# Kernel tuning notes

Hardware: AMD Instinct MI355X
Metric: run time of the kernel (lower is better)

The kernel has to match this reference:

```python
import jax, jax.numpy as jnp
import numpy as np

N_NODES = 200000
N_EDGES = 400000
N_FEAT = 78
DIM = 128
N_LAYERS = 5
N_GRAPHS = 8192
BN_EPS = 1e-5


def setup_inputs() -> dict:
    key = jax.random.key(0)
    ks = jax.random.split(key, 20)
    s = 0.05
    inp = {
        "x": jax.random.normal(ks[0], (N_NODES, N_FEAT), dtype=jnp.float32),
        "edge_index": jax.random.randint(ks[1], (2, N_EDGES), 0, N_NODES, dtype=jnp.int64),
        "batch": jnp.sort(jax.random.randint(ks[2], (N_NODES,), 0, N_GRAPHS, dtype=jnp.int64)),
        "percent": 0,
        # ini_embed: Linear(F,D), ReLU, Linear(D,D)
        "ini_w1": jax.random.normal(ks[3], (N_FEAT, DIM), dtype=jnp.float32) * s,
        "ini_b1": jnp.zeros((DIM,), dtype=jnp.float32),
        "ini_w2": jax.random.normal(ks[4], (DIM, DIM), dtype=jnp.float32) * s,
        "ini_b2": jnp.zeros((DIM,), dtype=jnp.float32),
        # per-layer GIN MLPs (stacked over layers)
        "gin_w1": jax.random.normal(ks[5], (N_LAYERS, DIM, DIM), dtype=jnp.float32) * s,
        "gin_b1": jnp.zeros((N_LAYERS, DIM), dtype=jnp.float32),
        "gin_w2": jax.random.normal(ks[6], (N_LAYERS, DIM, DIM), dtype=jnp.float32) * s,
        "gin_b2": jnp.zeros((N_LAYERS, DIM), dtype=jnp.float32),
        # BatchNorm1d params per layer
        "bn_gamma": jnp.ones((N_LAYERS, DIM), dtype=jnp.float32),
        "bn_beta": jnp.zeros((N_LAYERS, DIM), dtype=jnp.float32),
        # layer_conv: Conv2d(L, 1, (1,1)) == weighted sum over layer axis + scalar bias
        "lc_w": jax.random.normal(ks[7], (N_LAYERS,), dtype=jnp.float32) * s,
        "lc_b": jnp.zeros((), dtype=jnp.float32),
    }
    return inp


def reference(x, edge_index, batch, percent, ini_w1, ini_b1, ini_w2, ini_b2,
              gin_w1, gin_b1, gin_w2, gin_b2, bn_gamma, bn_beta, lc_w, lc_b):
    # ini_embed
    h = jax.nn.relu(x @ ini_w1 + ini_b1) @ ini_w2 + ini_b2  # [N, D]
    src, dst = edge_index[0], edge_index[1]

    layer_outs = []
    for i in range(N_LAYERS):
        # GINConv (eps=0): mlp(x_i + sum_{j->i} x_j)
        agg = jax.ops.segment_sum(h[src], dst, num_segments=N_NODES)  # scatter-add
        z = agg + h
        z = jax.nn.relu(z @ gin_w1[i] + gin_b1[i]) @ gin_w2[i] + gin_b2[i]
        z = jax.nn.relu(z)
        # BatchNorm1d (training-mode batch stats over nodes)
        mean = jnp.mean(z, axis=0)
        var = jnp.var(z, axis=0)
        z = (z - mean) * jax.lax.rsqrt(var + BN_EPS) * bn_gamma[i] + bn_beta[i]
        layer_outs.append(z)
        h = z

    stacked = jnp.stack(layer_outs, axis=1)  # [N, L, D]
    # layer_conv: 1x1 Conv2d over the layer channel axis
    pos_global_node = jnp.einsum('nld,l->nd', stacked, lc_w) + lc_b  # [N, D]
    # global_add_pool
    pos_global_graph = jax.ops.segment_sum(pos_global_node, batch, num_segments=N_GRAPHS)
    return pos_global_graph
```

## Files before the change

### kernel.cpp

```cpp
#include <hip/hip_runtime.h>

#define NN 200000
#define NE 400000
#define NFEAT 78
#define DIM 128
#define NLAYERS 5
#define NGRAPHS 8192
#define BN_EPS_C 1e-5f
#define NSLOT 32

typedef __attribute__((ext_vector_type(8))) short short8;
typedef __attribute__((ext_vector_type(8))) unsigned short ushort8;
typedef __attribute__((ext_vector_type(4))) float f32x4;

__device__ inline float bf2f(unsigned short u) {
    union { unsigned int i; float f; } c; c.i = ((unsigned int)u) << 16; return c.f;
}
__device__ inline unsigned short f2bf(float f) {
    union { float f; unsigned int i; } c; c.f = f;
    unsigned int x = c.i;
    x += 0x7FFFu + ((x >> 16) & 1u);
    return (unsigned short)(x >> 16);
}

template<int RELU2, int STATS>
__global__ __launch_bounds__(256, 2) void gin_mlp_kernel(
    const unsigned short* __restrict__ A,
    const unsigned short* __restrict__ W1sw, const unsigned short* __restrict__ W2sw,
    const float* __restrict__ b1, const float* __restrict__ b2,
    unsigned short* __restrict__ Z, float* __restrict__ stats_base)
{
    __shared__ unsigned short Abuf[16 * 128 * 8];
    __shared__ unsigned short Wbuf[16 * 128 * 8];
    __shared__ float sst[256];

    int t = threadIdx.x;
    int r0 = blockIdx.x * 128;
    int lane = t & 63;
    int wv = t >> 6;
    int l15 = lane & 15;
    int lg = lane >> 4;

#pragma unroll
    for (int it = 0; it < 8; ++it) {
        int flat = it * 256 + t;
        int kg = flat & 15, m = flat >> 4;
        int r = r0 + m;
        ushort8 v;
#pragma unroll
        for (int i = 0; i < 8; ++i) v[i] = 0;
        if (r < NN) v = *(const ushort8*)(A + (size_t)r * DIM + kg * 8);
        *(ushort8*)&Abuf[(kg * 128 + (m ^ (kg & 7))) * 8] = v;
        int idx = flat * 8;
        *(ushort8*)&Wbuf[idx] = *(const ushort8*)(W1sw + idx);
    }
    __syncthreads();

    float b1v[8], b2v[8];
#pragma unroll
    for (int nt = 0; nt < 8; ++nt) { b1v[nt] = b1[nt * 16 + l15]; b2v[nt] = b2[nt * 16 + l15]; }

    f32x4 zero4 = {0.f, 0.f, 0.f, 0.f};
    f32x4 acc[2][8];
#pragma unroll
    for (int mt = 0; mt < 2; ++mt)
#pragma unroll
        for (int nt = 0; nt < 8; ++nt) acc[mt][nt] = zero4;

#pragma unroll
    for (int ks = 0; ks < 4; ++ks) {
        int kgp = ks * 4 + lg;
        short8 a0 = *(const short8*)&Abuf[(kgp * 128 + ((wv * 32 + l15) ^ (kgp & 7))) * 8];
        short8 a1 = *(const short8*)&Abuf[(kgp * 128 + ((wv * 32 + 16 + l15) ^ (kgp & 7))) * 8];
#pragma unroll
        for (int nt = 0; nt < 8; ++nt) {
            short8 b = *(const short8*)&Wbuf[(kgp * 128 + ((nt * 16 + l15) ^ (kgp & 7))) * 8];
            acc[0][nt] = __builtin_amdgcn_mfma_f32_16x16x32_bf16(a0, b, acc[0][nt], 0, 0, 0);
            acc[1][nt] = __builtin_amdgcn_mfma_f32_16x16x32_bf16(a1, b, acc[1][nt], 0, 0, 0);
        }
    }
    __syncthreads();

#pragma unroll
    for (int mt = 0; mt < 2; ++mt)
#pragma unroll
        for (int nt = 0; nt < 8; ++nt)
#pragma unroll
            for (int rg = 0; rg < 4; ++rg) {
                int rr = wv * 32 + mt * 16 + lg * 4 + rg;
                int c = nt * 16 + l15;
                float v = fmaxf(acc[mt][nt][rg] + b1v[nt], 0.f);
                unsigned byte = (unsigned)((rr * 128 + c) * 2) ^ (unsigned)((rr & 7) << 4);
                *(unsigned short*)((char*)Abuf + byte) = f2bf(v);
            }
#pragma unroll
    for (int it = 0; it < 8; ++it) {
        int idx = (it * 256 + t) * 8;
        *(ushort8*)&Wbuf[idx] = *(const ushort8*)(W2sw + idx);
    }
    __syncthreads();

    f32x4 acc2[2][8];
#pragma unroll
    for (int mt = 0; mt < 2; ++mt)
#pragma unroll
        for (int nt = 0; nt < 8; ++nt) acc2[mt][nt] = zero4;

#pragma unroll
    for (int ks = 0; ks < 4; ++ks) {
        int kgp = ks * 4 + lg;
        int m0 = wv * 32 + l15, m1 = m0 + 16;
        unsigned ba0 = (unsigned)(m0 * 256 + kgp * 16) ^ (unsigned)((m0 & 7) << 4);
        unsigned ba1 = (unsigned)(m1 * 256 + kgp * 16) ^ (unsigned)((m1 & 7) << 4);
        short8 a0 = *(const short8*)((char*)Abuf + ba0);
        short8 a1 = *(const short8*)((char*)Abuf + ba1);
#pragma unroll
        for (int nt = 0; nt < 8; ++nt) {
            short8 b = *(const short8*)&Wbuf[(kgp * 128 + ((nt * 16 + l15) ^ (kgp & 7))) * 8];
            acc2[0][nt] = __builtin_amdgcn_mfma_f32_16x16x32_bf16(a0, b, acc2[0][nt], 0, 0, 0);
            acc2[1][nt] = __builtin_amdgcn_mfma_f32_16x16x32_bf16(a1, b, acc2[1][nt], 0, 0, 0);
        }
    }

    if (STATS) {
        sst[t] = 0.f;
        __syncthreads();
    }

#pragma unroll
    for (int nt = 0; nt < 8; ++nt) {
        float sum8 = 0.f, sq8 = 0.f;
        int c = nt * 16 + l15;
#pragma unroll
        for (int mt = 0; mt < 2; ++mt)
#pragma unroll
            for (int rg = 0; rg < 4; ++rg) {
                int rr = wv * 32 + mt * 16 + lg * 4 + rg;
                int r = r0 + rr;
                if (r < NN) {
                    float v = acc2[mt][nt][rg] + b2v[nt];
                    if (RELU2) v = fmaxf(v, 0.f);
                    Z[(size_t)r * DIM + c] = f2bf(v);
                    if (STATS) { sum8 += v; sq8 += v * v; }
                }
            }
        if (STATS) {
            atomicAdd(&sst[c], sum8);
            atomicAdd(&sst[128 + c], sq8);
        }
    }
    if (STATS) {
        __syncthreads();
        atomicAdd(&stats_base[(blockIdx.x & (NSLOT - 1)) * 256 + t], sst[t]);
    }
}

__global__ __launch_bounds__(256) void wconv_kernel(
    const float* __restrict__ ini_w1, const float* __restrict__ ini_w2,
    const float* __restrict__ gw1, const float* __restrict__ gw2,
    unsigned short* __restrict__ Wsw)
{
    int id = blockIdx.x * 256 + threadIdx.x;
    int k = id >> 7, n = id & 127;
    int y = blockIdx.y;
    float v;
    if (y == 0)      v = (k < NFEAT) ? ini_w1[k * DIM + n] : 0.f;
    else if (y == 1) v = ini_w2[k * DIM + n];
    else if (y < 7)  v = gw1[(size_t)(y - 2) * DIM * DIM + k * DIM + n];
    else             v = gw2[(size_t)(y - 7) * DIM * DIM + k * DIM + n];
    int kg = k >> 3;
    Wsw[(size_t)y * 16384 + (size_t)(kg * 128 + (n ^ (kg & 7))) * 8 + (k & 7)] = f2bf(v);
}

__global__ __launch_bounds__(256) void xpad_kernel(
    const float* __restrict__ x, unsigned short* __restrict__ xp)
{
    int t = blockIdx.x * 256 + threadIdx.x;
    int n = t >> 4, j = t & 15;
    ushort8 o;
#pragma unroll
    for (int i = 0; i < 8; ++i) {
        int c = j * 8 + i;
        o[i] = (c < NFEAT) ? f2bf(x[(size_t)n * NFEAT + c]) : (unsigned short)0;
    }
    *(ushort8*)(xp + (size_t)n * DIM + j * 8) = o;
}

__global__ __launch_bounds__(256) void deg_kernel(const int* __restrict__ ei, int* __restrict__ deg)
{
    int e = blockIdx.x * 256 + threadIdx.x;
    if (e >= NE) return;
    atomicAdd(&deg[ei[NE + e]], 1);
}

__global__ __launch_bounds__(256) void scanA_kernel(
    const int* __restrict__ deg, int* __restrict__ cursor, int* __restrict__ partials)
{
    __shared__ int sh[256];
    int i = blockIdx.x * 256 + threadIdx.x;
    int v = (i < NN) ? deg[i] : 0;
    sh[threadIdx.x] = v;
    __syncthreads();
    for (int off = 1; off < 256; off <<= 1) {
        int t2 = (threadIdx.x >= off) ? sh[threadIdx.x - off] : 0;
        __syncthreads();
        sh[threadIdx.x] += t2;
        __syncthreads();
    }
    int incl = sh[threadIdx.x];
    if (i < NN) cursor[i] = incl - v;
    if (threadIdx.x == 255) partials[blockIdx.x] = incl;
}

__global__ __launch_bounds__(1024) void scanB_kernel(int* __restrict__ partials, int nb)
{
    __shared__ int sh[1024];
    int i = threadIdx.x;
    int v = (i < nb) ? partials[i] : 0;
    sh[i] = v;
    __syncthreads();
    for (int off = 1; off < 1024; off <<= 1) {
        int t2 = (i >= off) ? sh[i - off] : 0;
        __syncthreads();
        sh[i] += t2;
        __syncthreads();
    }
    if (i < nb) partials[i] = sh[i] - v;
}

__global__ __launch_bounds__(256) void scanC_kernel(
    int* __restrict__ cursor, const int* __restrict__ partials)
{
    int i = blockIdx.x * 256 + threadIdx.x;
    if (i < NN) cursor[i] += partials[blockIdx.x];
}

__global__ __launch_bounds__(256) void fill_kernel(
    const int* __restrict__ ei, int* __restrict__ cursor, int* __restrict__ csr_src)
{
    int e = blockIdx.x * 256 + threadIdx.x;
    if (e >= NE) return;
    int slot = atomicAdd(&cursor[ei[NE + e]], 1);
    csr_src[slot] = ei[e];
}

__global__ __launch_bounds__(256) void gptr_kernel(
    const int* __restrict__ batch, int* __restrict__ gptr)
{
    int n = blockIdx.x * 256 + threadIdx.x;
    if (n > NN) return;
    int b1 = (n < NN) ? batch[n] : NGRAPHS;
    int b0 = (n == 0) ? -1 : batch[n - 1];
    for (int g = b0 + 1; g <= b1; ++g) gptr[g] = n;
}

__global__ void ident_kernel(float* __restrict__ aff)
{
    int d = threadIdx.x;
    aff[d] = 1.f;
    aff[DIM + d] = 0.f;
}

__global__ __launch_bounds__(256) void gather_kernel(
    const unsigned short* __restrict__ z, const int* __restrict__ cursor,
    const int* __restrict__ csr_src, const float* __restrict__ aff,
    unsigned short* __restrict__ agg)
{
    int t = blockIdx.x * 256 + threadIdx.x;
    int n = t >> 4, j = t & 15;
    int end = cursor[n];
    int beg = (n == 0) ? 0 : cursor[n - 1];
    ushort8 sv = *(const ushort8*)(z + (size_t)n * DIM + j * 8);
    float a[8];
#pragma unroll
    for (int i = 0; i < 8; ++i) a[i] = bf2f(sv[i]);
    for (int e = beg; e < end; ++e) {
        int s = csr_src[e];
        ushort8 v = *(const ushort8*)(z + (size_t)s * DIM + j * 8);
#pragma unroll
        for (int i = 0; i < 8; ++i) a[i] += bf2f(v[i]);
    }
    float cnt = (float)(end - beg + 1);
    ushort8 o;
#pragma unroll
    for (int i = 0; i < 8; ++i) {
        float av = aff[j * 8 + i];
        float cv = aff[DIM + j * 8 + i];
        o[i] = f2bf(fmaf(av, a[i], cnt * cv));
    }
    *(ushort8*)(agg + (size_t)n * DIM + j * 8) = o;
}

__global__ __launch_bounds__(128) void pool_kernel(
    const unsigned short* __restrict__ z, const int* __restrict__ gptr,
    const float* __restrict__ aff, const float* __restrict__ lcw, int l,
    const float* __restrict__ lcb_p, int add_lcb, float* __restrict__ out)
{
    int g = blockIdx.x;
    int d = threadIdx.x;
    int p0 = gptr[g], p1 = gptr[g + 1];
    float S = 0.f;
    for (int n = p0; n < p1; ++n) S += bf2f(z[(size_t)n * DIM + d]);
    float w = lcw[l];
    float cnt = (float)(p1 - p0);
    float v = w * fmaf(aff[d], S, cnt * aff[DIM + d]);
    if (add_lcb) v = fmaf(cnt, *lcb_p, v);
    out[(size_t)g * DIM + d] += v;
}

__global__ void finalize_kernel(
    const float* __restrict__ slots, const float* __restrict__ gamma,
    const float* __restrict__ beta, float* __restrict__ aff)
{
    int d = threadIdx.x;
    float s = 0.f, sq = 0.f;
    for (int i = 0; i < NSLOT; ++i) {
        s  += slots[i * 256 + d];
        sq += slots[i * 256 + 128 + d];
    }
    float mean = s * (1.0f / NN);
    float var = sq * (1.0f / NN) - mean * mean;
    float a = gamma[d] * rsqrtf(var + BN_EPS_C);
    aff[d] = a;
    aff[DIM + d] = beta[d] - mean * a;
}

extern "C" void kernel_launch(void* const* d_in, const int* in_sizes, int n_in,
                              void* d_out, int out_size, void* d_ws, size_t ws_size,
                              hipStream_t stream)
{
    const float* x      = (const float*)d_in[0];
    const int*   ei     = (const int*)d_in[1];
    const int*   batch  = (const int*)d_in[2];
    const float* ini_w1 = (const float*)d_in[4];
    const float* ini_b1 = (const float*)d_in[5];
    const float* ini_w2 = (const float*)d_in[6];
    const float* ini_b2 = (const float*)d_in[7];
    const float* gw1    = (const float*)d_in[8];
    const float* gb1    = (const float*)d_in[9];
    const float* gw2    = (const float*)d_in[10];
    const float* gb2    = (const float*)d_in[11];
    const float* gamma  = (const float*)d_in[12];
    const float* beta   = (const float*)d_in[13];
    const float* lcw    = (const float*)d_in[14];
    const float* lcb    = (const float*)d_in[15];
    float* out = (float*)d_out;

    size_t NHs = (size_t)NN * DIM;
    unsigned short* bufA = (unsigned short*)d_ws;
    unsigned short* bufB = bufA + NHs;
    unsigned short* Wsw  = bufB + NHs;
    float* stats  = (float*)(Wsw + 12 * 16384);
    float* affine = stats + (size_t)NLAYERS * NSLOT * 256;
    int* deg      = (int*)(affine + (NLAYERS + 1) * 256);
    int* cursor   = deg + NN;
    int* csr_src  = cursor + NN;
    int* partials = csr_src + NE;
    int* gptr     = partials + 1024;
    size_t need = (size_t)((char*)(gptr + NGRAPHS + 1) - (char*)d_ws);

    hipMemsetAsync(out, 0, (size_t)NGRAPHS * DIM * sizeof(float), stream);
    if (ws_size < need) return;

    hipMemsetAsync(stats, 0, (size_t)NLAYERS * NSLOT * 256 * sizeof(float), stream);
    hipMemsetAsync(deg, 0, NN * sizeof(int), stream);

    int nb = (NN + 255) / 256;
    int eb = (NE + 255) / 256;

    deg_kernel<<<eb, 256, 0, stream>>>(ei, deg);
    scanA_kernel<<<nb, 256, 0, stream>>>(deg, cursor, partials);
    scanB_kernel<<<1, 1024, 0, stream>>>(partials, nb);
    scanC_kernel<<<nb, 256, 0, stream>>>(cursor, partials);
    fill_kernel<<<eb, 256, 0, stream>>>(ei, cursor, csr_src);
    gptr_kernel<<<(NN + 256) / 256 + 1, 256, 0, stream>>>(batch, gptr);
    ident_kernel<<<1, 128, 0, stream>>>(affine);

    xpad_kernel<<<NN * 16 / 256, 256, 0, stream>>>(x, bufB);
    wconv_kernel<<<dim3(64, 12), 256, 0, stream>>>(ini_w1, ini_w2, gw1, gw2, Wsw);

    int gin_blocks = (NN + 127) / 128;

    gin_mlp_kernel<0, 0><<<gin_blocks, 256, 0, stream>>>(
        bufB, Wsw, Wsw + 16384, ini_b1, ini_b2, bufA, nullptr);

    unsigned short* prev = bufA;
    for (int l = 0; l < NLAYERS; ++l) {
        unsigned short* nxt = (prev == bufA) ? bufB : bufA;
        gather_kernel<<<NN * 16 / 256, 256, 0, stream>>>(
            prev, cursor, csr_src, affine + (size_t)l * 256, nxt);
        gin_mlp_kernel<1, 1><<<gin_blocks, 256, 0, stream>>>(
            nxt, Wsw + (size_t)(2 + l) * 16384, Wsw + (size_t)(7 + l) * 16384,
            gb1 + l * DIM, gb2 + l * DIM, nxt, stats + (size_t)l * NSLOT * 256);
        finalize_kernel<<<1, 128, 0, stream>>>(
            stats + (size_t)l * NSLOT * 256, gamma + l * DIM, beta + l * DIM,
            affine + (size_t)(l + 1) * 256);
        pool_kernel<<<NGRAPHS, 128, 0, stream>>>(
            nxt, gptr, affine + (size_t)(l + 1) * 256, lcw, l, lcb,
            (l == 0) ? 1 : 0, out);
        prev = nxt;
    }
}
```

Baseline: 781.7 us.

## Read GIN MLP operands directly from global memory and cut LDS usage

The fused two-layer MLP kernel no longer stages the activation tile and weight matrices in shared memory. Each wave loads its A rows and the weight fragments straight from global memory, which relies on L1/L2 caching of the weights; only the intermediate hidden tile stays in LDS. This removes the staging barriers and shrinks LDS so the launch bound can rise to 4 blocks per CU. BatchNorm stats are now reduced with wave shuffles and written with global atomics instead of LDS atomics, which raises the number of global atomics per block and may add contention on the stats slots.

After: 754.5 us. -3.5%, faster.

```diff
diff --git a/kernel.cpp b/kernel.cpp
--- a/kernel.cpp
+++ b/kernel.cpp
@@ -24,15 +24,13 @@
 }
 
 template<int RELU2, int STATS>
-__global__ __launch_bounds__(256, 2) void gin_mlp_kernel(
+__global__ __launch_bounds__(256, 4) void gin_mlp_kernel(
     const unsigned short* __restrict__ A,
-    const unsigned short* __restrict__ W1sw, const unsigned short* __restrict__ W2sw,
+    const unsigned short* __restrict__ W1d, const unsigned short* __restrict__ W2d,
     const float* __restrict__ b1, const float* __restrict__ b2,
     unsigned short* __restrict__ Z, float* __restrict__ stats_base)
 {
-    __shared__ unsigned short Abuf[16 * 128 * 8];
-    __shared__ unsigned short Wbuf[16 * 128 * 8];
-    __shared__ float sst[256];
+    __shared__ unsigned short C1[128 * 128];
 
     int t = threadIdx.x;
     int r0 = blockIdx.x * 128;
@@ -41,24 +39,14 @@
     int l15 = lane & 15;
     int lg = lane >> 4;
 
-#pragma unroll
-    for (int it = 0; it < 8; ++it) {
-        int flat = it * 256 + t;
-        int kg = flat & 15, m = flat >> 4;
-        int r = r0 + m;
-        ushort8 v;
-#pragma unroll
-        for (int i = 0; i < 8; ++i) v[i] = 0;
-        if (r < NN) v = *(const ushort8*)(A + (size_t)r * DIM + kg * 8);
-        *(ushort8*)&Abuf[(kg * 128 + (m ^ (kg & 7))) * 8] = v;
-        int idx = flat * 8;
-        *(ushort8*)&Wbuf[idx] = *(const ushort8*)(W1sw + idx);
-    }
-    __syncthreads();
-
     float b1v[8], b2v[8];
 #pragma unroll
     for (int nt = 0; nt < 8; ++nt) { b1v[nt] = b1[nt * 16 + l15]; b2v[nt] = b2[nt * 16 + l15]; }
+
+    int ra0 = r0 + wv * 32 + l15;       if (ra0 > NN - 1) ra0 = NN - 1;
+    int ra1 = r0 + wv * 32 + 16 + l15;  if (ra1 > NN - 1) ra1 = NN - 1;
+    const unsigned short* __restrict__ Arow0 = A + (size_t)ra0 * DIM;
+    const unsigned short* __restrict__ Arow1 = A + (size_t)ra1 * DIM;
 
     f32x4 zero4 = {0.f, 0.f, 0.f, 0.f};
     f32x4 acc[2][8];
@@ -70,16 +58,15 @@
 #pragma unroll
     for (int ks = 0; ks < 4; ++ks) {
         int kgp = ks * 4 + lg;
-        short8 a0 = *(const short8*)&Abuf[(kgp * 128 + ((wv * 32 + l15) ^ (kgp & 7))) * 8];
-        short8 a1 = *(const short8*)&Abuf[(kgp * 128 + ((wv * 32 + 16 + l15) ^ (kgp & 7))) * 8];
+        short8 a0 = *(const short8*)(Arow0 + kgp * 8);
+        short8 a1 = *(const short8*)(Arow1 + kgp * 8);
 #pragma unroll
         for (int nt = 0; nt < 8; ++nt) {
-            short8 b = *(const short8*)&Wbuf[(kgp * 128 + ((nt * 16 + l15) ^ (kgp & 7))) * 8];
+            short8 b = *(const short8*)(W1d + (size_t)(kgp * 128 + nt * 16 + l15) * 8);
             acc[0][nt] = __builtin_amdgcn_mfma_f32_16x16x32_bf16(a0, b, acc[0][nt], 0, 0, 0);
             acc[1][nt] = __builtin_amdgcn_mfma_f32_16x16x32_bf16(a1, b, acc[1][nt], 0, 0, 0);
         }
     }
-    __syncthreads();
 
 #pragma unroll
     for (int mt = 0; mt < 2; ++mt)
@@ -91,14 +78,8 @@
                 int c = nt * 16 + l15;
                 float v = fmaxf(acc[mt][nt][rg] + b1v[nt], 0.f);
                 unsigned byte = (unsigned)((rr * 128 + c) * 2) ^ (unsigned)((rr & 7) << 4);
-                *(unsigned short*)((char*)Abuf + byte) = f2bf(v);
+                *(unsigned short*)((char*)C1 + byte) = f2bf(v);
             }
-#pragma unroll
-    for (int it = 0; it < 8; ++it) {
-        int idx = (it * 256 + t) * 8;
-        *(ushort8*)&Wbuf[idx] = *(const ushort8*)(W2sw + idx);
-    }
-    __syncthreads();
 
     f32x4 acc2[2][8];
 #pragma unroll
@@ -112,19 +93,14 @@
         int m0 = wv * 32 + l15, m1 = m0 + 16;
         unsigned ba0 = (unsigned)(m0 * 256 + kgp * 16) ^ (unsigned)((m0 & 7) << 4);
         unsigned ba1 = (unsigned)(m1 * 256 + kgp * 16) ^ (unsigned)((m1 & 7) << 4);
-        short8 a0 = *(const short8*)((char*)Abuf + ba0);
-        short8 a1 = *(const short8*)((char*)Abuf + ba1);
+        short8 a0 = *(const short8*)((char*)C1 + ba0);
+        short8 a1 = *(const short8*)((char*)C1 + ba1);
 #pragma unroll
         for (int nt = 0; nt < 8; ++nt) {
-            short8 b = *(const short8*)&Wbuf[(kgp * 128 + ((nt * 16 + l15) ^ (kgp & 7))) * 8];
+            short8 b = *(const short8*)(W2d + (size_t)(kgp * 128 + nt * 16 + l15) * 8);
             acc2[0][nt] = __builtin_amdgcn_mfma_f32_16x16x32_bf16(a0, b, acc2[0][nt], 0, 0, 0);
             acc2[1][nt] = __builtin_amdgcn_mfma_f32_16x16x32_bf16(a1, b, acc2[1][nt], 0, 0, 0);
         }
-    }
-
-    if (STATS) {
-        sst[t] = 0.f;
-        __syncthreads();
     }
 
 #pragma unroll
@@ -145,20 +121,21 @@
                 }
             }
         if (STATS) {
-            atomicAdd(&sst[c], sum8);
-            atomicAdd(&sst[128 + c], sq8);
+            sum8 += __shfl_xor(sum8, 16); sum8 += __shfl_xor(sum8, 32);
+            sq8  += __shfl_xor(sq8, 16);  sq8  += __shfl_xor(sq8, 32);
+            if (lg == 0) {
+                float* sb = stats_base + (size_t)(blockIdx.x & (NSLOT - 1)) * 256;
+                atomicAdd(&sb[c], sum8);
+                atomicAdd(&sb[128 + c], sq8);
+            }
         }
-    }
-    if (STATS) {
-        __syncthreads();
-        atomicAdd(&stats_base[(blockIdx.x & (NSLOT - 1)) * 256 + t], sst[t]);
     }
 }
 
 __global__ __launch_bounds__(256) void wconv_kernel(
     const float* __restrict__ ini_w1, const float* __restrict__ ini_w2,
     const float* __restrict__ gw1, const float* __restrict__ gw2,
-    unsigned short* __restrict__ Wsw)
+    unsigned short* __restrict__ Wd)
 {
     int id = blockIdx.x * 256 + threadIdx.x;
     int k = id >> 7, n = id & 127;
@@ -169,7 +146,7 @@
     else if (y < 7)  v = gw1[(size_t)(y - 2) * DIM * DIM + k * DIM + n];
     else             v = gw2[(size_t)(y - 7) * DIM * DIM + k * DIM + n];
     int kg = k >> 3;
-    Wsw[(size_t)y * 16384 + (size_t)(kg * 128 + (n ^ (kg & 7))) * 8 + (k & 7)] = f2bf(v);
+    Wd[(size_t)y * 16384 + (size_t)(kg * 128 + n) * 8 + (k & 7)] = f2bf(v);
 }
 
 __global__ __launch_bounds__(256) void xpad_kernel(
@@ -349,8 +326,8 @@
     size_t NHs = (size_t)NN * DIM;
     unsigned short* bufA = (unsigned short*)d_ws;
     unsigned short* bufB = bufA + NHs;
-    unsigned short* Wsw  = bufB + NHs;
-    float* stats  = (float*)(Wsw + 12 * 16384);
+    unsigned short* Wd   = bufB + NHs;
+    float* stats  = (float*)(Wd + 12 * 16384);
     float* affine = stats + (size_t)NLAYERS * NSLOT * 256;
     int* deg      = (int*)(affine + (NLAYERS + 1) * 256);
     int* cursor   = deg + NN;
@@ -377,12 +354,12 @@
     ident_kernel<<<1, 128, 0, stream>>>(affine);
 
     xpad_kernel<<<NN * 16 / 256, 256, 0, stream>>>(x, bufB);
-    wconv_kernel<<<dim3(64, 12), 256, 0, stream>>>(ini_w1, ini_w2, gw1, gw2, Wsw);
+    wconv_kernel<<<dim3(64, 12), 256, 0, stream>>>(ini_w1, ini_w2, gw1, gw2, Wd);
 
     int gin_blocks = (NN + 127) / 128;
 
     gin_mlp_kernel<0, 0><<<gin_blocks, 256, 0, stream>>>(
-        bufB, Wsw, Wsw + 16384, ini_b1, ini_b2, bufA, nullptr);
+        bufB, Wd, Wd + 16384, ini_b1, ini_b2, bufA, nullptr);
 
     unsigned short* prev = bufA;
     for (int l = 0; l < NLAYERS; ++l) {
@@ -390,7 +367,7 @@
         gather_kernel<<<NN * 16 / 256, 256, 0, stream>>>(
             prev, cursor, csr_src, affine + (size_t)l * 256, nxt);
         gin_mlp_kernel<1, 1><<<gin_blocks, 256, 0, stream>>>(
-            nxt, Wsw + (size_t)(2 + l) * 16384, Wsw + (size_t)(7 + l) * 16384,
+            nxt, Wd + (size_t)(2 + l) * 16384, Wd + (size_t)(7 + l) * 16384,
             gb1 + l * DIM, gb2 + l * DIM, nxt, stats + (size_t)l * NSLOT * 256);
         finalize_kernel<<<1, 128, 0, stream>>>(
             stats + (size_t)l * NSLOT * 256, gamma + l * DIM, beta + l * DIM,
```
